# Kernel tuning notes

Hardware: AMD Instinct MI355X
Metric: run time of the kernel (lower is better)

Reference implementation:

```python
import jax, jax.numpy as jnp
import numpy as np

B, L, H, N, DM = 16, 32768, 64, 16, 32


def setup_inputs() -> dict:
    key = jax.random.key(0)
    ks = jax.random.split(key, 16)
    inp = {}
    inp['x'] = jax.random.normal(ks[0], (B, L, H), dtype=jnp.float32)
    inp['control_parameters'] = jax.random.uniform(ks[1], (B, 2), dtype=jnp.float32)
    inp['W0'] = jax.random.normal(ks[2], (2, DM), dtype=jnp.float32) / np.sqrt(2.0)
    inp['b0'] = jnp.zeros((DM,), dtype=jnp.float32)
    inp['W1'] = jax.random.normal(ks[3], (DM, DM), dtype=jnp.float32) / np.sqrt(DM)
    inp['b1'] = jnp.zeros((DM,), dtype=jnp.float32)
    inp['W2'] = jax.random.normal(ks[4], (DM, DM), dtype=jnp.float32) / np.sqrt(DM)
    inp['b2'] = jnp.zeros((DM,), dtype=jnp.float32)
    # BlockV1 input linear
    inp['W_lin'] = jax.random.normal(ks[5], (H, H), dtype=jnp.float32) / np.sqrt(H)
    inp['b_lin'] = jnp.zeros((H,), dtype=jnp.float32)
    # DSSM / S4D parameters (S4D-Lin init)
    log_dt_min, log_dt_max = np.log(1e-3), np.log(1e-1)
    inp['log_dt'] = (log_dt_min + (log_dt_max - log_dt_min)
                     * jax.random.uniform(ks[6], (H,), dtype=jnp.float32))
    inp['A_re'] = -0.5 * jnp.ones((H, N), dtype=jnp.float32)
    inp['A_im'] = jnp.broadcast_to(np.pi * jnp.arange(N, dtype=jnp.float32), (H, N)).copy()
    inp['C_re'] = jax.random.normal(ks[7], (H, N), dtype=jnp.float32) / np.sqrt(2.0)
    inp['C_im'] = jax.random.normal(ks[8], (H, N), dtype=jnp.float32) / np.sqrt(2.0)
    inp['D'] = jax.random.normal(ks[9], (H,), dtype=jnp.float32)
    # FiLM: Linear(DM, 2*H) -> (gamma, beta)
    inp['W_film'] = jax.random.normal(ks[10], (DM, 2 * H), dtype=jnp.float32) / np.sqrt(DM)
    inp['b_film'] = jnp.zeros((2 * H,), dtype=jnp.float32)
    return inp


def _s4d_kernel(log_dt, A_re, A_im, C_re, C_im, length):
    # Diagonal SSM (S4D) convolution kernel via ZOH discretization.
    dt = jnp.exp(log_dt)[:, None]                      # [H,1]
    A = A_re + 1j * A_im                               # [H,N]
    dtA = dt * A                                       # [H,N]
    C = (C_re + 1j * C_im) * (jnp.exp(dtA) - 1.0) / A  # [H,N]
    t = jnp.arange(length, dtype=jnp.float32)          # [L]
    # Vandermonde: K[h,l] = 2 * Re( sum_n C[h,n] * exp(dtA[h,n])^l )
    vand = jnp.exp(dtA[:, :, None] * t)                # [H,N,L] complex
    return 2.0 * jnp.einsum('hn,hnl->hl', C, vand).real


def reference(x, control_parameters, W0, b0, W1, b1, W2, b2,
              W_lin, b_lin, log_dt, A_re, A_im, C_re, C_im, D,
              W_film, b_film):
    gelu = jax.nn.gelu
    # control-parameter MLP -> conditioning vector [B, DM]
    cond = gelu(control_parameters @ W0 + b0)
    cond = gelu(cond @ W1 + b1)
    cond = gelu(cond @ W2 + b2)
    # BlockV1: Linear + act
    h = gelu(x @ W_lin + b_lin)          # [B,L,H]
    u = jnp.swapaxes(h, 1, 2)            # [B,H,L]
    length = u.shape[-1]
    # S4D global convolution via FFT (linear, non-circular)
    K = _s4d_kernel(log_dt, A_re, A_im, C_re, C_im, length)   # [H,L]
    n = 2 * length
    Kf = jnp.fft.rfft(K, n=n)            # [H, n//2+1]
    uf = jnp.fft.rfft(u, n=n)            # [B,H, n//2+1]
    y = jnp.fft.irfft(uf * Kf, n=n)[..., :length] + D[:, None] * u  # [B,H,L]
    y = jnp.swapaxes(y, 1, 2)            # [B,L,H]
    # FiLM conditioning (no batch norm)
    gb = cond @ W_film + b_film          # [B, 2H]
    g, b = jnp.split(gb, 2, axis=-1)     # [B,H] each
    y = gelu(y * g[:, None, :] + b[:, None, :])
    # side-chain gate: elementwise multiply with input
    return x * y
```

## Files before the change

kernel.cpp:

```cpp
#include <hip/hip_runtime.h>
#include <hip/hip_bf16.h>
#include <math.h>

#define B_ 16
#define L_ 32768
#define H_ 64
#define N_ 16
#define DM_ 32
#define T_ 128
#define C_ 256
#define TS_ 16

typedef __attribute__((ext_vector_type(8))) short short8;
typedef __attribute__((ext_vector_type(4))) float floatx4;

__device__ __forceinline__ float fast_gelu(float v) {
    float z = fmaf(0.044715f * v, v * v, v) * 0.7978845608028654f;
#if __has_builtin(__builtin_amdgcn_exp2f) && __has_builtin(__builtin_amdgcn_rcpf)
    float e = __builtin_amdgcn_exp2f(z * 2.8853900817779268f);
    float t = 1.0f - 2.0f * __builtin_amdgcn_rcpf(e + 1.0f);
#else
    float t = tanhf(z);
#endif
    return 0.5f * v * (1.0f + t);
}

__device__ __forceinline__ unsigned short bf16_rne(float f) {
    unsigned u = __float_as_uint(f);
    return (unsigned short)((u + 0x7FFFu + ((u >> 16) & 1u)) >> 16);
}
__device__ __forceinline__ float bf16_tof(unsigned short h) {
    return __uint_as_float(((unsigned)h) << 16);
}
__device__ __forceinline__ void cvt8(const float* f, short8* hi, short8* lo) {
    union { unsigned u[4]; short8 s; } Hh, Ll;
    #pragma unroll
    for (int jp = 0; jp < 4; ++jp) {
        unsigned short h0 = bf16_rne(f[2*jp]), h1 = bf16_rne(f[2*jp+1]);
        Hh.u[jp] = (unsigned)h0 | ((unsigned)h1 << 16);
        float l0 = f[2*jp]   - bf16_tof(h0);
        float l1 = f[2*jp+1] - bf16_tof(h1);
        Ll.u[jp] = (unsigned)bf16_rne(l0) | ((unsigned)bf16_rne(l1) << 16);
    }
    *hi = Hh.s; *lo = Ll.s;
}

__global__ void cond_film_kernel(const float* __restrict__ cp,
    const float* __restrict__ W0, const float* __restrict__ b0,
    const float* __restrict__ W1, const float* __restrict__ b1,
    const float* __restrict__ W2, const float* __restrict__ b2,
    const float* __restrict__ Wf, const float* __restrict__ bf,
    float* __restrict__ film) {
    __shared__ float ca[B_][DM_];
    __shared__ float cb[B_][DM_];
    int tid = threadIdx.x;
    int b = tid >> 5, j = tid & 31;
    float acc = fmaf(cp[b*2+0], W0[j], fmaf(cp[b*2+1], W0[DM_+j], b0[j]));
    ca[b][j] = fast_gelu(acc);
    __syncthreads();
    acc = b1[j];
    #pragma unroll
    for (int i = 0; i < DM_; ++i) acc = fmaf(ca[b][i], W1[i*DM_+j], acc);
    cb[b][j] = fast_gelu(acc);
    __syncthreads();
    acc = b2[j];
    #pragma unroll
    for (int i = 0; i < DM_; ++i) acc = fmaf(cb[b][i], W2[i*DM_+j], acc);
    float c2 = fast_gelu(acc);
    __syncthreads();
    ca[b][j] = c2;
    __syncthreads();
    #pragma unroll
    for (int t = 0; t < 4; ++t) {
        int k = j + DM_*t;
        float a = bf[k];
        #pragma unroll
        for (int i = 0; i < DM_; ++i) a = fmaf(ca[b][i], Wf[i*2*H_+k], a);
        film[b*2*H_ + k] = a;
    }
}

__global__ void coef_kernel(const float* __restrict__ log_dt,
    const float* __restrict__ A_re, const float* __restrict__ A_im,
    const float* __restrict__ C_re, const float* __restrict__ C_im,
    float* __restrict__ coef) {
    int g = blockIdx.x * blockDim.x + threadIdx.x;
    if (g >= H_*N_) return;
    int h = g >> 4, n = g & 15;
    float dt = expf(log_dt[h]);
    float Ar = A_re[h*N_+n], Ai = A_im[h*N_+n];
    float ar = dt*Ar, ai = dt*Ai;
    float er = expf(ar);
    float wr = er * cosf(ai), wi = er * sinf(ai);
    float eT = expf((float)T_ * ar);
    float aT = (float)T_ * ai;
    float wTr = eT * cosf(aT), wTi = eT * sinf(aT);
    float d  = Ar*Ar + Ai*Ai;
    float nr = wr - 1.0f, ni = wi;
    float qr = (nr*Ar + ni*Ai) / d;
    float qi = (ni*Ar - nr*Ai) / d;
    float Cr = C_re[h*N_+n], Ci = C_im[h*N_+n];
    float cr = 2.0f * (Cr*qr - Ci*qi);
    float ci = 2.0f * (Cr*qi + Ci*qr);
    coef[(n*6+0)*H_+h] = wr;
    coef[(n*6+1)*H_+h] = wi;
    coef[(n*6+2)*H_+h] = wTr;
    coef[(n*6+3)*H_+h] = wTi;
    coef[(n*6+4)*H_+h] = cr;
    coef[(n*6+5)*H_+h] = ci;
}

__global__ void chunk_scan_kernel(float* __restrict__ states,
                                  const float* __restrict__ coef) {
    int t = blockIdx.x * blockDim.x + threadIdx.x;
    int h = t & 63, n = (t >> 6) & 15, b = t >> 10;
    float wTr = coef[(n*6+2)*H_+h], wTi = coef[(n*6+3)*H_+h];
    float2* sp = (float2*)states + ((size_t)b*C_)*N_*H_ + (size_t)n*H_ + h;
    const int stride = N_*H_;
    float car = 0.f, cai = 0.f;
    float2 buf[8];
    #pragma unroll
    for (int i = 0; i < 8; ++i) buf[i] = sp[(size_t)i*stride];
    for (int cg = 0; cg < C_; cg += 8) {
        float2 nb[8];
        #pragma unroll
        for (int i = 0; i < 8; ++i)
            nb[i] = (cg + 8 + i < C_) ? sp[(size_t)(cg+8+i)*stride]
                                      : make_float2(0.f, 0.f);
        #pragma unroll
        for (int i = 0; i < 8; ++i) {
            float2 v = buf[i];
            sp[(size_t)(cg+i)*stride] = make_float2(car, cai);
            float nr2 = fmaf(wTr, car, fmaf(-wTi, cai, v.x));
            float ni2 = fmaf(wTr, cai, fmaf( wTi, car, v.y));
            car = nr2; cai = ni2;
            buf[i] = nb[i];
        }
    }
}

template<int PHASE>
__global__ __launch_bounds__(256, 3)
void gemm_scan_kernel(const float* __restrict__ x,
                      const float* __restrict__ W_lin, const float* __restrict__ b_lin,
                      const float* __restrict__ coef, float* __restrict__ states,
                      const float* __restrict__ D, const float* __restrict__ film,
                      float* __restrict__ out) {
    __shared__ __align__(16) unsigned short Wf[16*64*8];
    __shared__ float uld[4][TS_*65];
    const int lane = threadIdx.x & 63;
    const int wv   = threadIdx.x >> 6;
    const int q    = blockIdx.x*4 + wv;
    const int b    = q >> 8;
    const int c    = q & 255;
    const int m    = lane & 15;
    const int quad = lane >> 4;

    for (int kt = 0; kt < 2; ++kt)
        for (int nt = 0; nt < 4; ++nt) {
            float f[8];
            #pragma unroll
            for (int j = 0; j < 8; ++j)
                f[j] = W_lin[(kt*32 + quad*8 + j)*H_ + nt*16 + m];
            short8 hi, lo;
            cvt8(f, &hi, &lo);
            ((short8*)Wf)[(kt*4 + nt)*64 + lane]     = hi;
            ((short8*)Wf)[((2+kt)*4 + nt)*64 + lane] = lo;
        }

    float wr[N_], wi[N_], sr[N_], si[N_];
    float cr[N_], ci[N_];
    float g_ = 0.f, be_ = 0.f, Dh = 0.f;
    #pragma unroll
    for (int n = 0; n < N_; ++n) {
        wr[n] = coef[(n*6+0)*H_ + lane];
        wi[n] = coef[(n*6+1)*H_ + lane];
    }
    if (PHASE == 1) {
        #pragma unroll
        for (int n = 0; n < N_; ++n) { sr[n] = 0.f; si[n] = 0.f; }
    } else {
        #pragma unroll
        for (int n = 0; n < N_; ++n) {
            cr[n] = coef[(n*6+4)*H_ + lane];
            ci[n] = coef[(n*6+5)*H_ + lane];
            size_t idx = (((size_t)q*N_ + n)*H_ + lane)*2;
            sr[n] = states[idx]; si[n] = states[idx+1];
        }
        g_  = film[b*2*H_ + lane];
        be_ = film[b*2*H_ + H_ + lane];
        Dh  = D[lane];
    }
    float blv[4];
    #pragma unroll
    for (int nt = 0; nt < 4; ++nt) blv[nt] = b_lin[nt*16 + m];

    const float* xp = x + ((size_t)b*L_ + (size_t)c*T_)*H_;
    float* op = out + ((size_t)b*L_ + (size_t)c*T_)*H_;
    float* myu = uld[wv];

    for (int s = 0; s < T_/TS_; ++s) {
        const float* xs = xp + s*TS_*H_;
        short8 ah[2], al[2];
        #pragma unroll
        for (int kt = 0; kt < 2; ++kt) {
            const float* src = xs + m*H_ + kt*32 + quad*8;
            float4 v0 = *(const float4*)(src);
            float4 v1 = *(const float4*)(src + 4);
            float f[8] = {v0.x, v0.y, v0.z, v0.w, v1.x, v1.y, v1.z, v1.w};
            cvt8(f, &ah[kt], &al[kt]);
        }
        #pragma unroll
        for (int nt = 0; nt < 4; ++nt) {
            floatx4 acc = {0.f, 0.f, 0.f, 0.f};
            #pragma unroll
            for (int kt = 0; kt < 2; ++kt) {
                short8 bh = ((short8*)Wf)[(kt*4 + nt)*64 + lane];
                short8 bl = ((short8*)Wf)[((2+kt)*4 + nt)*64 + lane];
                acc = __builtin_amdgcn_mfma_f32_16x16x32_bf16(ah[kt], bh, acc, 0, 0, 0);
                acc = __builtin_amdgcn_mfma_f32_16x16x32_bf16(al[kt], bh, acc, 0, 0, 0);
                acc = __builtin_amdgcn_mfma_f32_16x16x32_bf16(ah[kt], bl, acc, 0, 0, 0);
            }
            #pragma unroll
            for (int r = 0; r < 4; ++r) {
                int row = quad*4 + r;
                float uv = fast_gelu(acc[r] + blv[nt]);
                myu[row*65 + nt*16 + m] = uv;
            }
        }
        for (int l = 0; l < TS_; ++l) {
            float uv = myu[l*65 + lane];
            if (PHASE == 1) {
                #pragma unroll
                for (int n = 0; n < N_; ++n) {
                    float nr = fmaf(wr[n], sr[n], fmaf(-wi[n], si[n], uv));
                    float ni = fmaf(wr[n], si[n], wi[n]*sr[n]);
                    sr[n] = nr; si[n] = ni;
                }
            } else {
                float xg = xs[l*H_ + lane];
                float y0 = 0.f, y1 = 0.f;
                #pragma unroll
                for (int n = 0; n < N_; ++n) {
                    float nr = fmaf(wr[n], sr[n], fmaf(-wi[n], si[n], uv));
                    float ni = fmaf(wr[n], si[n], wi[n]*sr[n]);
                    sr[n] = nr; si[n] = ni;
                    y0 = fmaf(cr[n], nr, y0);
                    y1 = fmaf(ci[n], ni, y1);
                }
                float y  = fmaf(Dh, uv, y0 - y1);
                float yg = fast_gelu(fmaf(y, g_, be_));
                op[(s*TS_ + l)*H_ + lane] = xg * yg;
            }
        }
    }
    if (PHASE == 1) {
        #pragma unroll
        for (int n = 0; n < N_; ++n) {
            size_t idx = (((size_t)q*N_ + n)*H_ + lane)*2;
            states[idx]   = sr[n];
            states[idx+1] = si[n];
        }
    }
}

extern "C" void kernel_launch(void* const* d_in, const int* in_sizes, int n_in,
                              void* d_out, int out_size, void* d_ws, size_t ws_size,
                              hipStream_t stream) {
    const float* x     = (const float*)d_in[0];
    const float* cp    = (const float*)d_in[1];
    const float* W0    = (const float*)d_in[2];
    const float* b0    = (const float*)d_in[3];
    const float* W1    = (const float*)d_in[4];
    const float* b1    = (const float*)d_in[5];
    const float* W2    = (const float*)d_in[6];
    const float* b2    = (const float*)d_in[7];
    const float* W_lin = (const float*)d_in[8];
    const float* b_lin = (const float*)d_in[9];
    const float* log_dt= (const float*)d_in[10];
    const float* A_re  = (const float*)d_in[11];
    const float* A_im  = (const float*)d_in[12];
    const float* C_re  = (const float*)d_in[13];
    const float* C_im  = (const float*)d_in[14];
    const float* D     = (const float*)d_in[15];
    const float* W_f   = (const float*)d_in[16];
    const float* b_f   = (const float*)d_in[17];
    float* out = (float*)d_out;

    float* film   = (float*)d_ws;
    float* coef   = film + B_*2*H_;
    float* states = coef + 6*H_*N_;

    cond_film_kernel<<<1, 512, 0, stream>>>(cp, W0, b0, W1, b1, W2, b2,
                                            W_f, b_f, film);
    coef_kernel<<<4, 256, 0, stream>>>(log_dt, A_re, A_im, C_re, C_im, coef);
    gemm_scan_kernel<1><<<(B_*C_)/4, 256, 0, stream>>>(x, W_lin, b_lin, coef,
                                                       states, nullptr, nullptr, nullptr);
    chunk_scan_kernel<<<(B_*N_*H_)/256, 256, 0, stream>>>(states, coef);
    gemm_scan_kernel<3><<<(B_*C_)/4, 256, 0, stream>>>(x, W_lin, b_lin, coef,
                                                       states, D, film, out);
}
```

Before: 546.9 us.

## Merge prep kernels, precompute split-bf16 weights, prefetch x tiles and stage via LDS

```diff
diff --git a/kernel.cpp b/kernel.cpp
--- a/kernel.cpp
+++ b/kernel.cpp
@@ -10,9 +10,11 @@
 #define T_ 128
 #define C_ 256
 #define TS_ 16
+#define STR_ 68
 
 typedef __attribute__((ext_vector_type(8))) short short8;
 typedef __attribute__((ext_vector_type(4))) float floatx4;
+typedef unsigned short ushort_t;
 
 __device__ __forceinline__ float fast_gelu(float v) {
     float z = fmaf(0.044715f * v, v * v, v) * 0.7978845608028654f;
@@ -45,69 +47,98 @@
     *hi = Hh.s; *lo = Ll.s;
 }
 
-__global__ void cond_film_kernel(const float* __restrict__ cp,
+__global__ void prep_kernel(const float* __restrict__ cp,
     const float* __restrict__ W0, const float* __restrict__ b0,
     const float* __restrict__ W1, const float* __restrict__ b1,
     const float* __restrict__ W2, const float* __restrict__ b2,
-    const float* __restrict__ Wf, const float* __restrict__ bf,
-    float* __restrict__ film) {
-    __shared__ float ca[B_][DM_];
-    __shared__ float cb[B_][DM_];
-    int tid = threadIdx.x;
-    int b = tid >> 5, j = tid & 31;
-    float acc = fmaf(cp[b*2+0], W0[j], fmaf(cp[b*2+1], W0[DM_+j], b0[j]));
-    ca[b][j] = fast_gelu(acc);
-    __syncthreads();
-    acc = b1[j];
-    #pragma unroll
-    for (int i = 0; i < DM_; ++i) acc = fmaf(ca[b][i], W1[i*DM_+j], acc);
-    cb[b][j] = fast_gelu(acc);
-    __syncthreads();
-    acc = b2[j];
-    #pragma unroll
-    for (int i = 0; i < DM_; ++i) acc = fmaf(cb[b][i], W2[i*DM_+j], acc);
-    float c2 = fast_gelu(acc);
-    __syncthreads();
-    ca[b][j] = c2;
-    __syncthreads();
-    #pragma unroll
-    for (int t = 0; t < 4; ++t) {
-        int k = j + DM_*t;
-        float a = bf[k];
-        #pragma unroll
-        for (int i = 0; i < DM_; ++i) a = fmaf(ca[b][i], Wf[i*2*H_+k], a);
-        film[b*2*H_ + k] = a;
-    }
-}
-
-__global__ void coef_kernel(const float* __restrict__ log_dt,
+    const float* __restrict__ Wfilm, const float* __restrict__ bfilm,
+    const float* __restrict__ W_lin,
+    const float* __restrict__ log_dt,
     const float* __restrict__ A_re, const float* __restrict__ A_im,
     const float* __restrict__ C_re, const float* __restrict__ C_im,
-    float* __restrict__ coef) {
-    int g = blockIdx.x * blockDim.x + threadIdx.x;
-    if (g >= H_*N_) return;
-    int h = g >> 4, n = g & 15;
-    float dt = expf(log_dt[h]);
-    float Ar = A_re[h*N_+n], Ai = A_im[h*N_+n];
-    float ar = dt*Ar, ai = dt*Ai;
-    float er = expf(ar);
-    float wr = er * cosf(ai), wi = er * sinf(ai);
-    float eT = expf((float)T_ * ar);
-    float aT = (float)T_ * ai;
-    float wTr = eT * cosf(aT), wTi = eT * sinf(aT);
-    float d  = Ar*Ar + Ai*Ai;
-    float nr = wr - 1.0f, ni = wi;
-    float qr = (nr*Ar + ni*Ai) / d;
-    float qi = (ni*Ar - nr*Ai) / d;
-    float Cr = C_re[h*N_+n], Ci = C_im[h*N_+n];
-    float cr = 2.0f * (Cr*qr - Ci*qi);
-    float ci = 2.0f * (Cr*qi + Ci*qr);
-    coef[(n*6+0)*H_+h] = wr;
-    coef[(n*6+1)*H_+h] = wi;
-    coef[(n*6+2)*H_+h] = wTr;
-    coef[(n*6+3)*H_+h] = wTi;
-    coef[(n*6+4)*H_+h] = cr;
-    coef[(n*6+5)*H_+h] = ci;
+    float* __restrict__ film, float* __restrict__ coef, ushort_t* __restrict__ gWf) {
+    int tid = threadIdx.x;
+    if (blockIdx.x == 0) {
+        __shared__ float ca[B_][DM_];
+        __shared__ float cb[B_][DM_];
+        int b = tid >> 4, jj = tid & 15;
+        #pragma unroll
+        for (int t = 0; t < 2; ++t) {
+            int j = jj + 16*t;
+            float acc = fmaf(cp[b*2+0], W0[j], fmaf(cp[b*2+1], W0[DM_+j], b0[j]));
+            ca[b][j] = fast_gelu(acc);
+        }
+        __syncthreads();
+        #pragma unroll
+        for (int t = 0; t < 2; ++t) {
+            int j = jj + 16*t;
+            float acc = b1[j];
+            #pragma unroll
+            for (int i = 0; i < DM_; ++i) acc = fmaf(ca[b][i], W1[i*DM_+j], acc);
+            cb[b][j] = fast_gelu(acc);
+        }
+        __syncthreads();
+        float c2[2];
+        #pragma unroll
+        for (int t = 0; t < 2; ++t) {
+            int j = jj + 16*t;
+            float acc = b2[j];
+            #pragma unroll
+            for (int i = 0; i < DM_; ++i) acc = fmaf(cb[b][i], W2[i*DM_+j], acc);
+            c2[t] = fast_gelu(acc);
+        }
+        __syncthreads();
+        #pragma unroll
+        for (int t = 0; t < 2; ++t) ca[b][jj+16*t] = c2[t];
+        __syncthreads();
+        #pragma unroll
+        for (int t = 0; t < 8; ++t) {
+            int k = jj + 16*t;
+            float a = bfilm[k];
+            #pragma unroll
+            for (int i = 0; i < DM_; ++i) a = fmaf(ca[b][i], Wfilm[i*2*H_+k], a);
+            film[b*2*H_ + k] = a;
+        }
+    } else if (blockIdx.x == 1) {
+        for (int it = 0; it < 4; ++it) {
+            int g = tid + 256*it;
+            int h = g >> 4, n = g & 15;
+            float dt = expf(log_dt[h]);
+            float Ar = A_re[h*N_+n], Ai = A_im[h*N_+n];
+            float ar = dt*Ar, ai = dt*Ai;
+            float er = expf(ar);
+            float wr = er * cosf(ai), wi = er * sinf(ai);
+            float eT = expf((float)T_ * ar);
+            float aT = (float)T_ * ai;
+            float wTr = eT * cosf(aT), wTi = eT * sinf(aT);
+            float d  = Ar*Ar + Ai*Ai;
+            float nr = wr - 1.0f, ni = wi;
+            float qr = (nr*Ar + ni*Ai) / d;
+            float qi = (ni*Ar - nr*Ai) / d;
+            float Cr = C_re[h*N_+n], Ci = C_im[h*N_+n];
+            float cr = 2.0f * (Cr*qr - Ci*qi);
+            float ci = 2.0f * (Cr*qi + Ci*qr);
+            coef[(n*6+0)*H_+h] = wr;
+            coef[(n*6+1)*H_+h] = wi;
+            coef[(n*6+2)*H_+h] = wTr;
+            coef[(n*6+3)*H_+h] = wTi;
+            coef[(n*6+4)*H_+h] = cr;
+            coef[(n*6+5)*H_+h] = ci;
+        }
+    } else {
+        int lane = tid & 63, grp = tid >> 6;
+        int m = lane & 15, quad = lane >> 4;
+        for (int f = grp*4; f < grp*4 + 4; ++f) {
+            int t = f >> 3, kt = (f >> 2) & 1, nt = f & 3;
+            float fv[8];
+            #pragma unroll
+            for (int j = 0; j < 8; ++j)
+                fv[j] = W_lin[(kt*32 + quad*8 + j)*H_ + nt*16 + m];
+            short8 hi, lo;
+            cvt8(fv, &hi, &lo);
+            ((short8*)gWf)[f*64 + lane] = t ? lo : hi;
+        }
+    }
 }
 
 __global__ void chunk_scan_kernel(float* __restrict__ states,
@@ -115,20 +146,20 @@
     int t = blockIdx.x * blockDim.x + threadIdx.x;
     int h = t & 63, n = (t >> 6) & 15, b = t >> 10;
     float wTr = coef[(n*6+2)*H_+h], wTi = coef[(n*6+3)*H_+h];
-    float2* sp = (float2*)states + ((size_t)b*C_)*N_*H_ + (size_t)n*H_ + h;
+    float2* sp = (float2*)states + (size_t)b*C_*N_*H_ + (size_t)n*H_ + h;
     const int stride = N_*H_;
     float car = 0.f, cai = 0.f;
-    float2 buf[8];
+    float2 buf[16];
     #pragma unroll
-    for (int i = 0; i < 8; ++i) buf[i] = sp[(size_t)i*stride];
-    for (int cg = 0; cg < C_; cg += 8) {
-        float2 nb[8];
-        #pragma unroll
-        for (int i = 0; i < 8; ++i)
-            nb[i] = (cg + 8 + i < C_) ? sp[(size_t)(cg+8+i)*stride]
-                                      : make_float2(0.f, 0.f);
-        #pragma unroll
-        for (int i = 0; i < 8; ++i) {
+    for (int i = 0; i < 16; ++i) buf[i] = sp[(size_t)i*stride];
+    for (int cg = 0; cg < C_; cg += 16) {
+        float2 nb[16];
+        #pragma unroll
+        for (int i = 0; i < 16; ++i)
+            nb[i] = (cg + 16 + i < C_) ? sp[(size_t)(cg+16+i)*stride]
+                                       : make_float2(0.f, 0.f);
+        #pragma unroll
+        for (int i = 0; i < 16; ++i) {
             float2 v = buf[i];
             sp[(size_t)(cg+i)*stride] = make_float2(car, cai);
             float nr2 = fmaf(wTr, car, fmaf(-wTi, cai, v.x));
@@ -140,33 +171,34 @@
 }
 
 template<int PHASE>
-__global__ __launch_bounds__(256, 3)
+__global__ __launch_bounds__(256, PHASE == 1 ? 4 : 3)
 void gemm_scan_kernel(const float* __restrict__ x,
-                      const float* __restrict__ W_lin, const float* __restrict__ b_lin,
+                      const ushort_t* __restrict__ gWf,
+                      const float* __restrict__ b_lin,
                       const float* __restrict__ coef, float* __restrict__ states,
                       const float* __restrict__ D, const float* __restrict__ film,
                       float* __restrict__ out) {
-    __shared__ __align__(16) unsigned short Wf[16*64*8];
-    __shared__ float uld[4][TS_*65];
-    const int lane = threadIdx.x & 63;
-    const int wv   = threadIdx.x >> 6;
-    const int q    = blockIdx.x*4 + wv;
-    const int b    = q >> 8;
-    const int c    = q & 255;
-    const int m    = lane & 15;
+    extern __shared__ char smem[];
+    short8* Wf   = (short8*)smem;
+    float*  uBase = (float*)(smem + 16384);
+    const int tid  = threadIdx.x;
+    const int lane = tid & 63;
+    const int wv   = tid >> 6;
+    float* myu = uBase + wv * (TS_*STR_);
+    float* xt  = uBase + 4*(TS_*STR_) + wv*(TS_*STR_);
+
+    {
+        const short8* src = (const short8*)gWf;
+        #pragma unroll
+        for (int i = 0; i < 4; ++i) Wf[i*256 + tid] = src[i*256 + tid];
+    }
+    __syncthreads();
+
+    const int q = blockIdx.x*4 + wv;
+    const int b = q >> 8;
+    const int c = q & 255;
+    const int m = lane & 15;
     const int quad = lane >> 4;
-
-    for (int kt = 0; kt < 2; ++kt)
-        for (int nt = 0; nt < 4; ++nt) {
-            float f[8];
-            #pragma unroll
-            for (int j = 0; j < 8; ++j)
-                f[j] = W_lin[(kt*32 + quad*8 + j)*H_ + nt*16 + m];
-            short8 hi, lo;
-            cvt8(f, &hi, &lo);
-            ((short8*)Wf)[(kt*4 + nt)*64 + lane]     = hi;
-            ((short8*)Wf)[((2+kt)*4 + nt)*64 + lane] = lo;
-        }
 
     float wr[N_], wi[N_], sr[N_], si[N_];
     float cr[N_], ci[N_];
@@ -197,39 +229,52 @@
 
     const float* xp = x + ((size_t)b*L_ + (size_t)c*T_)*H_;
     float* op = out + ((size_t)b*L_ + (size_t)c*T_)*H_;
-    float* myu = uld[wv];
+    const float* a0 = xp + m*H_ + quad*8;
+
+    float4 p00 = *(const float4*)(a0);
+    float4 p01 = *(const float4*)(a0 + 4);
+    float4 p10 = *(const float4*)(a0 + 32);
+    float4 p11 = *(const float4*)(a0 + 36);
 
     for (int s = 0; s < T_/TS_; ++s) {
-        const float* xs = xp + s*TS_*H_;
+        float4 c00 = p00, c01 = p01, c10 = p10, c11 = p11;
+        if (s < T_/TS_ - 1) {
+            const float* nx = a0 + (size_t)(s+1)*TS_*H_;
+            p00 = *(const float4*)(nx);
+            p01 = *(const float4*)(nx + 4);
+            p10 = *(const float4*)(nx + 32);
+            p11 = *(const float4*)(nx + 36);
+        }
+        if (PHASE == 3) {
+            *(float4*)(xt + m*STR_ + quad*8)          = c00;
+            *(float4*)(xt + m*STR_ + quad*8 + 4)      = c01;
+            *(float4*)(xt + m*STR_ + 32 + quad*8)     = c10;
+            *(float4*)(xt + m*STR_ + 32 + quad*8 + 4) = c11;
+        }
         short8 ah[2], al[2];
-        #pragma unroll
-        for (int kt = 0; kt < 2; ++kt) {
-            const float* src = xs + m*H_ + kt*32 + quad*8;
-            float4 v0 = *(const float4*)(src);
-            float4 v1 = *(const float4*)(src + 4);
-            float f[8] = {v0.x, v0.y, v0.z, v0.w, v1.x, v1.y, v1.z, v1.w};
-            cvt8(f, &ah[kt], &al[kt]);
+        {
+            float f0[8] = {c00.x,c00.y,c00.z,c00.w,c01.x,c01.y,c01.z,c01.w};
+            cvt8(f0, &ah[0], &al[0]);
+            float f1[8] = {c10.x,c10.y,c10.z,c10.w,c11.x,c11.y,c11.z,c11.w};
+            cvt8(f1, &ah[1], &al[1]);
         }
         #pragma unroll
         for (int nt = 0; nt < 4; ++nt) {
             floatx4 acc = {0.f, 0.f, 0.f, 0.f};
             #pragma unroll
             for (int kt = 0; kt < 2; ++kt) {
-                short8 bh = ((short8*)Wf)[(kt*4 + nt)*64 + lane];
-                short8 bl = ((short8*)Wf)[((2+kt)*4 + nt)*64 + lane];
+                short8 bh = Wf[(kt*4 + nt)*64 + lane];
+                short8 bl = Wf[((2+kt)*4 + nt)*64 + lane];
                 acc = __builtin_amdgcn_mfma_f32_16x16x32_bf16(ah[kt], bh, acc, 0, 0, 0);
                 acc = __builtin_amdgcn_mfma_f32_16x16x32_bf16(al[kt], bh, acc, 0, 0, 0);
                 acc = __builtin_amdgcn_mfma_f32_16x16x32_bf16(ah[kt], bl, acc, 0, 0, 0);
             }
             #pragma unroll
-            for (int r = 0; r < 4; ++r) {
-                int row = quad*4 + r;
-                float uv = fast_gelu(acc[r] + blv[nt]);
-                myu[row*65 + nt*16 + m] = uv;
-            }
+            for (int r = 0; r < 4; ++r)
+                myu[(quad*4 + r)*STR_ + nt*16 + m] = fast_gelu(acc[r] + blv[nt]);
         }
         for (int l = 0; l < TS_; ++l) {
-            float uv = myu[l*65 + lane];
+            float uv = myu[l*STR_ + lane];
             if (PHASE == 1) {
                 #pragma unroll
                 for (int n = 0; n < N_; ++n) {
@@ -238,7 +283,7 @@
                     sr[n] = nr; si[n] = ni;
                 }
             } else {
-                float xg = xs[l*H_ + lane];
+                float xg = xt[l*STR_ + lane];
                 float y0 = 0.f, y1 = 0.f;
                 #pragma unroll
                 for (int n = 0; n < N_; ++n) {
@@ -287,16 +332,17 @@
     const float* b_f   = (const float*)d_in[17];
     float* out = (float*)d_out;
 
-    float* film   = (float*)d_ws;
-    float* coef   = film + B_*2*H_;
-    float* states = coef + 6*H_*N_;
-
-    cond_film_kernel<<<1, 512, 0, stream>>>(cp, W0, b0, W1, b1, W2, b2,
-                                            W_f, b_f, film);
-    coef_kernel<<<4, 256, 0, stream>>>(log_dt, A_re, A_im, C_re, C_im, coef);
-    gemm_scan_kernel<1><<<(B_*C_)/4, 256, 0, stream>>>(x, W_lin, b_lin, coef,
-                                                       states, nullptr, nullptr, nullptr);
+    float*    film   = (float*)d_ws;
+    float*    coef   = film + B_*2*H_;
+    ushort_t* gWf    = (ushort_t*)(coef + 6*H_*N_);
+    float*    states = (float*)(gWf + 16*64*8);
+
+    prep_kernel<<<3, 256, 0, stream>>>(cp, W0, b0, W1, b1, W2, b2, W_f, b_f,
+                                       W_lin, log_dt, A_re, A_im, C_re, C_im,
+                                       film, coef, gWf);
+    gemm_scan_kernel<1><<<(B_*C_)/4, 256, 16384 + 4*TS_*STR_*4, stream>>>(
+        x, gWf, b_lin, coef, states, nullptr, nullptr, nullptr);
     chunk_scan_kernel<<<(B_*N_*H_)/256, 256, 0, stream>>>(states, coef);
-    gemm_scan_kernel<3><<<(B_*C_)/4, 256, 0, stream>>>(x, W_lin, b_lin, coef,
-                                                       states, D, film, out);
-}
+    gemm_scan_kernel<3><<<(B_*C_)/4, 256, 16384 + 8*TS_*STR_*4, stream>>>(
+        x, gWf, b_lin, coef, states, D, film, out);
+}
```

New measurement: 556.6 us. Within noise of the previous version (+1.8%).
